# Performance work log

Measured on AMD Instinct MI355X. Metric: run time of the kernel, lower is better.

The kernel has to match this reference:

```python
import jax, jax.numpy as jnp
import numpy as np

THR = 1.0     # snntorch Leaky default threshold
BETA = 0.9    # args.beta
ALPHA = 2.0   # surrogate.atan default alpha

@jax.custom_vjp
def atan_spike(x):
    # Heaviside forward, arctan surrogate gradient (snntorch surrogate.atan)
    return (x > 0).astype(x.dtype)

def _aspk_fwd(x):
    return atan_spike(x), x

def _aspk_bwd(x, g):
    return (g * (ALPHA / 2.0) / (1.0 + (jnp.pi / 2.0 * ALPHA * x) ** 2),)

atan_spike.defvjp(_aspk_fwd, _aspk_bwd)

def setup_inputs() -> dict:
    key = jax.random.key(0)
    k = jax.random.split(key, 5)
    B, D, H, C = 32768, 187, 50, 5
    return {
        "x": jax.random.normal(k[0], (B, D), dtype=jnp.float32),
        "W1": jax.random.normal(k[1], (H, D), dtype=jnp.float32) * (1.0 / np.sqrt(D)),
        "b1": jax.random.normal(k[2], (H,), dtype=jnp.float32) * 0.01,
        "W2": jax.random.normal(k[3], (C, H), dtype=jnp.float32) * (1.0 / np.sqrt(H)),
        "b2": jax.random.normal(k[4], (C,), dtype=jnp.float32) * 0.01,
        "num_steps": 100,
    }

def reference(x, W1, b1, W2, b2, num_steps):
    B = x.shape[0]
    dt = x.dtype
    # fc1(x) is identical every timestep (x is static), compute once
    cur1 = x @ W1.T + b1  # [B, 50]

    def step(carry, _):
        mem1, mem2 = carry
        # Leaky: reset computed from PREVIOUS mem (detached), subtract mechanism
        reset1 = jax.lax.stop_gradient((mem1 > THR).astype(dt))
        mem1 = BETA * mem1 + cur1 - reset1 * THR
        spk1 = atan_spike(mem1 - THR)
        cur2 = spk1 @ W2.T + b2  # [B, num_classes]
        reset2 = jax.lax.stop_gradient((mem2 > THR).astype(dt))
        mem2 = BETA * mem2 + cur2 - reset2 * THR
        spk2 = atan_spike(mem2 - THR)
        return (mem1, mem2), (spk2, mem2)

    init = (jnp.zeros((B, W1.shape[0]), dt), jnp.zeros((B, W2.shape[0]), dt))
    _, (spk_rec, mem_rec) = jax.lax.scan(step, init, None, length=num_steps)
    return spk_rec, mem_rec  # each [num_steps, B, num_classes]
```

## Files before the change

kernel.cpp:

```cpp
#include <hip/hip_runtime.h>

typedef float v2f __attribute__((ext_vector_type(2)));

#define DD   187
#define HH   50
#define PH   56
#define HPJ  14
#define NP   7
#define NC   5
#define RPB  64
#define BLK  256
#define DCH  64
#define NCHUNK 3
#define BETA 0.9f

__device__ __forceinline__ float dpp_xor1(float v) {
    return __builtin_bit_cast(float,
        __builtin_amdgcn_mov_dpp(__builtin_bit_cast(int, v), 0xB1, 0xF, 0xF, true));
}
__device__ __forceinline__ float dpp_xor2(float v) {
    return __builtin_bit_cast(float,
        __builtin_amdgcn_mov_dpp(__builtin_bit_cast(int, v), 0x4E, 0xF, 0xF, true));
}

__device__ __forceinline__ float spike1(float m) {
    float t = fmaf(m, 0x1.0p60f, -0x1.0p60f);
    return fminf(fmaxf(t, 0.f), 1.f);
}
__device__ __forceinline__ v2f spike2(v2f m) {
    const v2f BIG2  = { 0x1.0p60f,  0x1.0p60f};
    const v2f NBIG2 = {-0x1.0p60f, -0x1.0p60f};
    const v2f ONE2  = {1.f, 1.f};
    const v2f ZERO2 = {0.f, 0.f};
    v2f t = __builtin_elementwise_fma(m, BIG2, NBIG2);
    return __builtin_elementwise_min(__builtin_elementwise_max(t, ZERO2), ONE2);
}

__global__ __launch_bounds__(BLK, 2)
void snn_kernel(const float* __restrict__ x,
                const float* __restrict__ W1,
                const float* __restrict__ b1,
                const float* __restrict__ W2,
                const float* __restrict__ b2,
                const int*   __restrict__ nsp,
                float* __restrict__ out, int Brows)
{
    __shared__ float xs[RPB * 65];
    __shared__ float w1t[DCH * PH];

    const int tid = threadIdx.x;
    const int p   = tid >> 2;
    const int k   = tid & 3;
    const int row = blockIdx.x * RPB + p;
    const int NS  = nsp[0];

    v2f acc[NP];
#pragma unroll
    for (int i = 0; i < NP; ++i) acc[i] = (v2f){0.f, 0.f};

    for (int ch = 0; ch < NCHUNK; ++ch) {
        const int d0 = ch * DCH;
        for (int i = tid; i < RPB * DCH; i += BLK) {
            int r = i >> 6, dd = i & 63;
            int d = d0 + dd;
            xs[r * 65 + dd] = (d < DD) ? x[(size_t)(blockIdx.x * RPB + r) * DD + d] : 0.f;
        }
        for (int i = tid; i < DCH * PH; i += BLK) {
            int h = i >> 6, dd = i & 63;
            int d = d0 + dd;
            w1t[dd * PH + h] = (h < HH && d < DD) ? W1[h * DD + d] : 0.f;
        }
        __syncthreads();

        const float* xr = xs + p * 65;
#pragma unroll 4
        for (int d = 0; d < DCH; ++d) {
            float xv = xr[d];
            const v2f* wr = (const v2f*)(w1t + d * PH + k * HPJ);
            v2f xvv = {xv, xv};
#pragma unroll
            for (int i = 0; i < NP; ++i)
                acc[i] = __builtin_elementwise_fma(xvv, wr[i], acc[i]);
        }
        __syncthreads();
    }

    v2f c1[NP];
#pragma unroll
    for (int i = 0; i < NP; ++i) {
        int h0 = k * HPJ + 2 * i;
        v2f bb = { (h0     < HH) ? b1[h0]     : 0.f,
                   (h0 + 1 < HH) ? b1[h0 + 1] : 0.f };
        c1[i] = acc[i] + bb;
    }

    v2f w2r[NC][NP];
#pragma unroll
    for (int c = 0; c < NC; ++c)
#pragma unroll
        for (int i = 0; i < NP; ++i) {
            int h0 = k * HPJ + 2 * i;
            w2r[c][i] = { (h0     < HH) ? W2[c * HH + h0]     : 0.f,
                          (h0 + 1 < HH) ? W2[c * HH + h0 + 1] : 0.f };
        }
    const float b2A = b2[k];
    const float b2B = b2[4];

    v2f m1[NP], s1[NP];
#pragma unroll
    for (int i = 0; i < NP; ++i) { m1[i] = (v2f){0.f, 0.f}; s1[i] = (v2f){0.f, 0.f}; }
    float mA = 0.f, sA = 0.f, mB = 0.f, sB = 0.f;

    const size_t stride = (size_t)Brows * NC;
    float* spkBase = out;
    float* memBase = out + (size_t)NS * stride;
    const int offA = row * NC + k;
    const int offB = row * NC + 4;
    const v2f BETA2 = {BETA, BETA};

    for (int t = 0; t < NS; ++t) {
        v2f cp[NC];
#pragma unroll
        for (int c = 0; c < NC; ++c) cp[c] = (v2f){0.f, 0.f};
#pragma unroll
        for (int i = 0; i < NP; ++i) {
            v2f m = __builtin_elementwise_fma(BETA2, m1[i], c1[i]) - s1[i];
            m1[i] = m;
            v2f s = spike2(m);
            s1[i] = s;
#pragma unroll
            for (int c = 0; c < NC; ++c)
                cp[c] = __builtin_elementwise_fma(s, w2r[c][i], cp[c]);
        }
        float cur2[NC];
#pragma unroll
        for (int c = 0; c < NC; ++c) {
            float r = cp[c].x + cp[c].y;
            r += dpp_xor1(r);
            r += dpp_xor2(r);
            cur2[c] = r;
        }
        float cA = (k == 0) ? cur2[0] : (k == 1) ? cur2[1] : (k == 2) ? cur2[2] : cur2[3];
        float cB = cur2[4];

        mA = fmaf(BETA, mA, cA + b2A) - sA;
        sA = spike1(mA);
        mB = fmaf(BETA, mB, cB + b2B) - sB;
        sB = spike1(mB);

        spkBase[offA] = sA;
        memBase[offA] = mA;
        if (k == 0) { spkBase[offB] = sB; memBase[offB] = mB; }

        spkBase += stride;
        memBase += stride;
    }
}

extern "C" void kernel_launch(void* const* d_in, const int* in_sizes, int n_in,
                              void* d_out, int out_size, void* d_ws, size_t ws_size,
                              hipStream_t stream) {
    const float* x  = (const float*)d_in[0];
    const float* W1 = (const float*)d_in[1];
    const float* b1 = (const float*)d_in[2];
    const float* W2 = (const float*)d_in[3];
    const float* b2 = (const float*)d_in[4];
    const int*   ns = (const int*)d_in[5];
    int B = in_sizes[0] / DD;
    int nblocks = B / RPB;
    snn_kernel<<<nblocks, BLK, 0, stream>>>(x, W1, b1, W2, b2, ns, (float*)d_out, B);
}
```

Baseline: 215.9 us.

## Stage per-step outputs in LDS and write them out as coalesced vector stores

Each block now buffers the spike and membrane outputs for groups of 16 timesteps in shared memory, reusing the x/W1 staging area. After each group it writes them to global memory as contiguous float4 stores, replacing the scattered per-thread scalar stores made every step. This adds two block-wide barriers per group and more LDS use (40 KB), which may lower occupancy.

```diff
diff --git a/kernel.cpp b/kernel.cpp
--- a/kernel.cpp
+++ b/kernel.cpp
@@ -1,6 +1,7 @@
 #include <hip/hip_runtime.h>
 
 typedef float v2f __attribute__((ext_vector_type(2)));
+typedef float f4  __attribute__((ext_vector_type(4)));
 
 #define DD   187
 #define HH   50
@@ -13,6 +14,9 @@
 #define DCH  64
 #define NCHUNK 3
 #define BETA 0.9f
+#define GRP  16
+#define SLAB (RPB * NC)
+#define LDSF (2 * GRP * SLAB)
 
 __device__ __forceinline__ float dpp_xor1(float v) {
     return __builtin_bit_cast(float,
@@ -45,13 +49,16 @@
                 const int*   __restrict__ nsp,
                 float* __restrict__ out, int Brows)
 {
-    __shared__ float xs[RPB * 65];
-    __shared__ float w1t[DCH * PH];
+    __shared__ alignas(16) float smem[LDSF];
+    float* xs  = smem;
+    float* w1t = smem + RPB * 65;
+    float* spk_lds = smem;
+    float* mem_lds = smem + GRP * SLAB;
 
     const int tid = threadIdx.x;
     const int p   = tid >> 2;
     const int k   = tid & 3;
-    const int row = blockIdx.x * RPB + p;
+    const int row0 = blockIdx.x * RPB;
     const int NS  = nsp[0];
 
     v2f acc[NP];
@@ -63,7 +70,7 @@
         for (int i = tid; i < RPB * DCH; i += BLK) {
             int r = i >> 6, dd = i & 63;
             int d = d0 + dd;
-            xs[r * 65 + dd] = (d < DD) ? x[(size_t)(blockIdx.x * RPB + r) * DD + d] : 0.f;
+            xs[r * 65 + dd] = (d < DD) ? x[(size_t)(row0 + r) * DD + d] : 0.f;
         }
         for (int i = tid; i < DCH * PH; i += BLK) {
             int h = i >> 6, dd = i & 63;
@@ -112,48 +119,69 @@
     float mA = 0.f, sA = 0.f, mB = 0.f, sB = 0.f;
 
     const size_t stride = (size_t)Brows * NC;
-    float* spkBase = out;
-    float* memBase = out + (size_t)NS * stride;
-    const int offA = row * NC + k;
-    const int offB = row * NC + 4;
+    const int p5k = p * NC + k;
     const v2f BETA2 = {BETA, BETA};
 
-    for (int t = 0; t < NS; ++t) {
-        v2f cp[NC];
-#pragma unroll
-        for (int c = 0; c < NC; ++c) cp[c] = (v2f){0.f, 0.f};
-#pragma unroll
-        for (int i = 0; i < NP; ++i) {
-            v2f m = __builtin_elementwise_fma(BETA2, m1[i], c1[i]) - s1[i];
-            m1[i] = m;
-            v2f s = spike2(m);
-            s1[i] = s;
-#pragma unroll
-            for (int c = 0; c < NC; ++c)
-                cp[c] = __builtin_elementwise_fma(s, w2r[c][i], cp[c]);
-        }
-        float cur2[NC];
-#pragma unroll
-        for (int c = 0; c < NC; ++c) {
-            float r = cp[c].x + cp[c].y;
-            r += dpp_xor1(r);
-            r += dpp_xor2(r);
-            cur2[c] = r;
-        }
-        float cA = (k == 0) ? cur2[0] : (k == 1) ? cur2[1] : (k == 2) ? cur2[2] : cur2[3];
-        float cB = cur2[4];
-
-        mA = fmaf(BETA, mA, cA + b2A) - sA;
-        sA = spike1(mA);
-        mB = fmaf(BETA, mB, cB + b2B) - sB;
-        sB = spike1(mB);
-
-        spkBase[offA] = sA;
-        memBase[offA] = mA;
-        if (k == 0) { spkBase[offB] = sB; memBase[offB] = mB; }
-
-        spkBase += stride;
-        memBase += stride;
+    __syncthreads();
+
+    int t0 = 0;
+    while (t0 < NS) {
+        const int steps = (NS - t0 < GRP) ? (NS - t0) : GRP;
+
+        for (int u = 0; u < steps; ++u) {
+            v2f cp[NC];
+#pragma unroll
+            for (int c = 0; c < NC; ++c) cp[c] = (v2f){0.f, 0.f};
+#pragma unroll
+            for (int i = 0; i < NP; ++i) {
+                v2f m = __builtin_elementwise_fma(BETA2, m1[i], c1[i]) - s1[i];
+                m1[i] = m;
+                v2f s = spike2(m);
+                s1[i] = s;
+#pragma unroll
+                for (int c = 0; c < NC; ++c)
+                    cp[c] = __builtin_elementwise_fma(s, w2r[c][i], cp[c]);
+            }
+            float cur2[NC];
+#pragma unroll
+            for (int c = 0; c < NC; ++c) {
+                float r = cp[c].x + cp[c].y;
+                r += dpp_xor1(r);
+                r += dpp_xor2(r);
+                cur2[c] = r;
+            }
+            float cA = (k == 0) ? cur2[0] : (k == 1) ? cur2[1] : (k == 2) ? cur2[2] : cur2[3];
+            float cB = cur2[4];
+
+            mA = fmaf(BETA, mA, cA + b2A) - sA;
+            sA = spike1(mA);
+            mB = fmaf(BETA, mB, cB + b2B) - sB;
+            sB = spike1(mB);
+
+            spk_lds[u * SLAB + p5k] = sA;
+            mem_lds[u * SLAB + p5k] = mA;
+            if (k == 0) {
+                spk_lds[u * SLAB + p * NC + 4] = sB;
+                mem_lds[u * SLAB + p * NC + 4] = mB;
+            }
+        }
+
+        __syncthreads();
+
+        const int totalChunks = steps * (SLAB / 4);
+        for (int c = tid; c < totalChunks; c += BLK) {
+            int u   = c / (SLAB / 4);
+            int pos = c - u * (SLAB / 4);
+            f4 sv = *(const f4*)(spk_lds + u * SLAB + pos * 4);
+            f4 mv = *(const f4*)(mem_lds + u * SLAB + pos * 4);
+            float* sp = out + (size_t)(t0 + u) * stride + (size_t)row0 * NC + pos * 4;
+            float* mp = sp + (size_t)NS * stride;
+            *(f4*)sp = sv;
+            *(f4*)mp = mv;
+        }
+
+        __syncthreads();
+        t0 += steps;
     }
 }
 
```

Measured after the change: 220.8 us. 2.3% more time.
